# Kernel tuning notes

Hardware: AMD Instinct MI355X
Metric: run time of the kernel (lower is better)

The kernel has to match this reference:

```python
import jax, jax.numpy as jnp
import numpy as np

D_MODEL = 1024
NUM_HEADS = 16
D_K = D_MODEL // NUM_HEADS


def setup_inputs() -> dict:
    key = jax.random.key(0)
    ks = jax.random.split(key, 9)
    s = 1.0 / np.sqrt(D_MODEL)
    x = jax.random.normal(ks[0], (2, 2048, D_MODEL), dtype=jnp.float32)
    Wq = jax.random.uniform(ks[1], (D_MODEL, D_MODEL), jnp.float32, -s, s)
    bq = jax.random.uniform(ks[2], (D_MODEL,), jnp.float32, -s, s)
    Wk = jax.random.uniform(ks[3], (D_MODEL, D_MODEL), jnp.float32, -s, s)
    bk = jax.random.uniform(ks[4], (D_MODEL,), jnp.float32, -s, s)
    Wv = jax.random.uniform(ks[5], (D_MODEL, D_MODEL), jnp.float32, -s, s)
    bv = jax.random.uniform(ks[6], (D_MODEL,), jnp.float32, -s, s)
    Wo = jax.random.uniform(ks[7], (D_MODEL, D_MODEL), jnp.float32, -s, s)
    bo = jax.random.uniform(ks[8], (D_MODEL,), jnp.float32, -s, s)
    return {"x": x, "Wq": Wq, "bq": bq, "Wk": Wk, "bk": bk,
            "Wv": Wv, "bv": bv, "Wo": Wo, "bo": bo}


def reference(x, Wq, bq, Wk, bk, Wv, bv, Wo, bo):
    B, S, _ = x.shape
    # projections (torch Linear: x @ W.T + b; here W stored as [in, out])
    q = (x @ Wq + bq).reshape(B, S, NUM_HEADS, D_K).transpose(0, 2, 1, 3)
    k = (x @ Wk + bk).reshape(B, S, NUM_HEADS, D_K).transpose(0, 2, 1, 3)
    v = (x @ Wv + bv).reshape(B, S, NUM_HEADS, D_K).transpose(0, 2, 1, 3)
    scores = jnp.einsum('bhqd,bhkd->bhqk', q, k) / jnp.sqrt(jnp.float32(D_K))
    attn = jax.nn.softmax(scores, axis=-1)
    out = jnp.einsum('bhqk,bhkd->bhqd', attn, v)  # [B,H,S,Dk]
    out = out.transpose(0, 2, 1, 3).reshape(B, S, D_MODEL)
    return out @ Wo + bo
```

## Files before the change

kernel.cpp:

```cpp
#include <hip/hip_runtime.h>
#include <hip/hip_bf16.h>

#define SEQ   2048
#define DM    1024
#define NH    16
#define DK    64
#define BATCH 2
#define M_TOT 4096
#define C1 0.18033688011112042f

typedef __attribute__((ext_vector_type(8))) short bf16x8;
typedef __attribute__((ext_vector_type(4))) float f32x4;
typedef __attribute__((ext_vector_type(16))) float f32x16;
typedef __attribute__((ext_vector_type(2))) int i32x2;
typedef unsigned short u16;

__device__ inline u16 f2b(float f) {
    union { float f; unsigned u; } x; x.f = f;
    return (u16)((x.u + 0x7FFFu + ((x.u >> 16) & 1u)) >> 16);
}

__device__ inline unsigned pk2(float a, float b) {
    __hip_bfloat162 h = __float22bfloat162_rn(make_float2(a, b));
    return *reinterpret_cast<unsigned*>(&h);
}

__device__ inline void async_cp16(const u16* g, u16* l) {
    __builtin_amdgcn_global_load_lds(
        (const __attribute__((address_space(1))) unsigned int*)g,
        (__attribute__((address_space(3))) unsigned int*)l, 16, 0, 0);
}

__device__ inline f32x16 zero16() {
    f32x16 z;
    #pragma unroll
    for (int i = 0; i < 16; ++i) z[i] = 0.f;
    return z;
}

__device__ inline bf16x8 mk8(unsigned a, unsigned b, unsigned c, unsigned d) {
    union { unsigned u[4]; bf16x8 v; } x;
    x.u[0] = a; x.u[1] = b; x.u[2] = c; x.u[3] = d;
    return x.v;
}

#define MFMA32(a, b, c) __builtin_amdgcn_mfma_f32_32x32x16_bf16(a, b, c, 0, 0, 0)

__global__ __launch_bounds__(256) void cast_x(
    const float4* __restrict__ x, uint2* __restrict__ xb)
{
    int gid = blockIdx.x * 256 + threadIdx.x;
    float4 v = x[gid];
    uint2 o;
    o.x = pk2(v.x, v.y); o.y = pk2(v.z, v.w);
    xb[gid] = o;
}

__global__ __launch_bounds__(256) void transpose_cast4(
    const float* __restrict__ W0, const float* __restrict__ W1,
    const float* __restrict__ W2, const float* __restrict__ W3,
    u16* __restrict__ WtBase)
{
    __shared__ float tile[32][33];
    const int t = threadIdx.x;
    const int n0 = blockIdx.x << 5, k0 = blockIdx.y << 5, z = blockIdx.z;
    const float* W = (z == 0) ? W0 : (z == 1) ? W1 : (z == 2) ? W2 : W3;
    u16* Wt = WtBase + (size_t)z * DM * DM;
    #pragma unroll
    for (int i = 0; i < 4; ++i) {
        int idx = t + (i << 8); int r = idx >> 5, c = idx & 31;
        tile[r][c] = W[(size_t)(k0 + r) * DM + n0 + c];
    }
    __syncthreads();
    #pragma unroll
    for (int i = 0; i < 4; ++i) {
        int idx = t + (i << 8); int r = idx >> 5, c = idx & 31;
        Wt[(size_t)(n0 + r) * DM + k0 + c] = f2b(tile[c][r]);
    }
}

__global__ __launch_bounds__(256) void gemm_bt(
    const u16* __restrict__ A, const u16* __restrict__ Bt, int mode,
    const float* __restrict__ bias0, const float* __restrict__ bias1,
    const float* __restrict__ bias2,
    void* __restrict__ out0, void* __restrict__ out1, void* __restrict__ out2)
{
    __shared__ u16 sh[9216];
    u16* As = sh;
    u16* Bs = sh + 4096;
    const int t = threadIdx.x, wid = t >> 6, lane = t & 63;
    const int lr = lane & 15, quad = lane >> 4;
    const int m0 = blockIdx.y << 7, n0 = blockIdx.x << 7;
    const int wm = (wid & 1) << 6, wn = (wid >> 1) << 6;
    const int rowA = lane >> 2;
    const int colA = (((lane & 3) - ((lane >> 3) & 3)) & 3) << 3;
    const int sA = (((lr >> 1) + quad) & 3) << 3;

    f32x4 acc[4][4];
    #pragma unroll
    for (int i = 0; i < 4; ++i)
        #pragma unroll
        for (int j = 0; j < 4; ++j) acc[i][j] = (f32x4){0.f, 0.f, 0.f, 0.f};

    for (int k0 = 0; k0 < DM; k0 += 32) {
        #pragma unroll
        for (int i = 0; i < 2; ++i) {
            int ch = wid * 2 + i;
            async_cp16(A  + (size_t)(m0 + ch * 16 + rowA) * DM + k0 + colA,
                       As + ch * 16 * 32);
            async_cp16(Bt + (size_t)(n0 + ch * 16 + rowA) * DM + k0 + colA,
                       Bs + ch * 16 * 32);
        }
        __syncthreads();
        bf16x8 af[4], bfr[4];
        #pragma unroll
        for (int mt = 0; mt < 4; ++mt)
            af[mt] = *(const bf16x8*)(As + (wm + 16 * mt + lr) * 32 + sA);
        #pragma unroll
        for (int nt = 0; nt < 4; ++nt)
            bfr[nt] = *(const bf16x8*)(Bs + (wn + 16 * nt + lr) * 32 + sA);
        #pragma unroll
        for (int mt = 0; mt < 4; ++mt)
            #pragma unroll
            for (int nt = 0; nt < 4; ++nt)
                acc[mt][nt] = __builtin_amdgcn_mfma_f32_16x16x32_bf16(
                    af[mt], bfr[nt], acc[mt][nt], 0, 0, 0);
        __syncthreads();
    }

    if (mode == 1) {
        u16* wstrip = sh + wid * 1152;
        const int ngb = n0 + wn;
        const int which = ngb >> 10, nnb = ngb & 1023;
        const int h = nnb >> 6;
        const float* bp = (which == 0) ? bias0 : (which == 1) ? bias1 : bias2;
        const float sc = (which == 0) ? C1 : 1.0f;
        float bias_v[4];
        #pragma unroll
        for (int nt = 0; nt < 4; ++nt) bias_v[nt] = bp[nnb + 16 * nt + lr];

        if (which != 1) {
            u16* dst = (which == 0) ? (u16*)out0 : (u16*)out2;
            #pragma unroll
            for (int mt = 0; mt < 4; ++mt) {
                #pragma unroll
                for (int nt = 0; nt < 4; ++nt) {
                    uint2 w;
                    w.x = pk2((acc[mt][nt][0] + bias_v[nt]) * sc,
                              (acc[mt][nt][1] + bias_v[nt]) * sc);
                    w.y = pk2((acc[mt][nt][2] + bias_v[nt]) * sc,
                              (acc[mt][nt][3] + bias_v[nt]) * sc);
                    *(uint2*)(wstrip + (16 * nt + lr) * 16 + quad * 4) = w;
                }
                asm volatile("s_waitcnt lgkmcnt(0)" ::: "memory");
                #pragma unroll
                for (int half = 0; half < 2; ++half) {
                    int id = lane + 64 * half;
                    int d = id >> 1, cho = (id & 1) << 3;
                    int m = m0 + wm + 16 * mt + cho;
                    int b = m >> 11, s = m & (SEQ - 1);
                    *(uint4*)(dst + ((size_t)(b * NH + h) * DK + d) * SEQ + s) =
                        *(const uint4*)(wstrip + d * 16 + cho);
                }
                asm volatile("s_waitcnt lgkmcnt(0)" ::: "memory");
            }
        } else {
            u16* dst = (u16*)out1;
            #pragma unroll
            for (int mt = 0; mt < 4; ++mt) {
                #pragma unroll
                for (int nt = 0; nt < 4; ++nt)
                    #pragma unroll
                    for (int r = 0; r < 4; ++r)
                        wstrip[(quad * 4 + r) * 72 + 16 * nt + lr] =
                            f2b(acc[mt][nt][r] + bias_v[nt]);
                asm volatile("s_waitcnt lgkmcnt(0)" ::: "memory");
                #pragma unroll
                for (int half = 0; half < 2; ++half) {
                    int id = lane + 64 * half;
                    int mloc = id >> 3, dl = (id & 7) << 3;
                    int m = m0 + wm + 16 * mt + mloc;
                    int b = m >> 11, s = m & (SEQ - 1);
                    *(uint4*)(dst + ((size_t)(b * NH + h) * SEQ + s) * DK + dl) =
                        *(const uint4*)(wstrip + mloc * 72 + dl);
                }
                asm volatile("s_waitcnt lgkmcnt(0)" ::: "memory");
            }
        }
    } else {
        float* O = (float*)out0;
        float* strip = (float*)sh + wid * 1088;
        float bias_v[4];
        #pragma unroll
        for (int nt = 0; nt < 4; ++nt) bias_v[nt] = bias0[n0 + wn + 16 * nt + lr];
        #pragma unroll
        for (int mt = 0; mt < 4; ++mt) {
            #pragma unroll
            for (int nt = 0; nt < 4; ++nt)
                #pragma unroll
                for (int r = 0; r < 4; ++r)
                    strip[(quad * 4 + r) * 68 + 16 * nt + lr] =
                        acc[mt][nt][r] + bias_v[nt];
            asm volatile("s_waitcnt lgkmcnt(0)" ::: "memory");
            #pragma unroll
            for (int rr = 0; rr < 4; ++rr) {
                int row = lane >> 2, chunk = (lane & 3) + 4 * rr;
                float4 v = *(const float4*)(strip + row * 68 + chunk * 4);
                *(float4*)(O + (size_t)(m0 + wm + 16 * mt + row) * DM
                             + n0 + wn + chunk * 4) = v;
            }
            asm volatile("s_waitcnt lgkmcnt(0)" ::: "memory");
        }
    }
}

__global__ __launch_bounds__(256) void attn_mfma(
    const u16* __restrict__ Qt, const u16* __restrict__ K,
    const u16* __restrict__ Vt, u16* __restrict__ A)
{
    __shared__ u16 sh[16640];

    const int t = threadIdx.x, wid = t >> 6, lane = t & 63;
    const int l31 = lane & 31, hi = lane >> 5, l7 = lane & 7;
    const int bx = blockIdx.x;
    const int xcd = bx & 7, within = bx >> 3;
    const int bh  = xcd * 4 + (within >> 4);
    const int q0  = (within & 15) << 7;

    const u16* Kb = K  + (size_t)bh * SEQ * DK;
    const u16* Vb = Vt + (size_t)bh * DK * SEQ;

    const int qw = q0 + 32 * wid + l31;
    const u16* Qb = Qt + (size_t)bh * DK * SEQ + qw;
    bf16x8 bQ[4];
    #pragma unroll
    for (int s = 0; s < 4; ++s)
        #pragma unroll
        for (int j = 0; j < 8; ++j)
            bQ[s][j] = (short)Qb[(size_t)(16 * s + 8 * hi + j) * SEQ];

    f32x16 O0 = zero16(), O1 = zero16();
    float lr = 0.f;

    const int srow = t >> 3;
    const int scol = (((t & 7) ^ (srow & 7)) << 3);

    const int rA = l31 * 64;
    int cks[4];
    #pragma unroll
    for (int s = 0; s < 4; ++s) cks[s] = ((2 * s + hi) ^ l7) << 3;

    auto stage = [&](int kt, int buf) {
        u16* kd = sh + (buf << 12);
        u16* vd = sh + 8192 + (buf << 12);
        async_cp16(Kb + (size_t)(kt + srow) * DK + scol,       kd + wid * 512);
        async_cp16(Kb + (size_t)(kt + srow + 32) * DK + scol,  kd + 2048 + wid * 512);
        async_cp16(Vb + (size_t)srow * SEQ + kt + scol,        vd + wid * 512);
        async_cp16(Vb + (size_t)(srow + 32) * SEQ + kt + scol, vd + 2048 + wid * 512);
    };

    stage(0, 0);
    __syncthreads();

    for (int it = 0; it < SEQ / 64; ++it) {
        const u16* kbp = sh + ((it & 1) << 12) + rA;
        const u16* vbp = sh + 8192 + ((it & 1) << 12) + rA;
        if (it + 1 < SEQ / 64) stage((it + 1) << 6, (it + 1) & 1);

        f32x16 Sv[2];
        __builtin_amdgcn_s_setprio(1);
        {
            bf16x8 a;
            f32x16 s0 = zero16();
            a = *(const bf16x8*)(kbp + cks[0]); s0 = MFMA32(a, bQ[0], s0);
            a = *(const bf16x8*)(kbp + cks[1]); s0 = MFMA32(a, bQ[1], s0);
            a = *(const bf16x8*)(kbp + cks[2]); s0 = MFMA32(a, bQ[2], s0);
            a = *(const bf16x8*)(kbp + cks[3]); s0 = MFMA32(a, bQ[3], s0);
            Sv[0] = s0;
            f32x16 s1 = zero16();
            a = *(const bf16x8*)(kbp + 2048 + cks[0]); s1 = MFMA32(a, bQ[0], s1);
            a = *(const bf16x8*)(kbp + 2048 + cks[1]); s1 = MFMA32(a, bQ[1], s1);
            a = *(const bf16x8*)(kbp + 2048 + cks[2]); s1 = MFMA32(a, bQ[2], s1);
            a = *(const bf16x8*)(kbp + 2048 + cks[3]); s1 = MFMA32(a, bQ[3], s1);
            Sv[1] = s1;
        }
        __builtin_amdgcn_s_setprio(0);

        unsigned pa[4][4];
        #pragma unroll
        for (int kvt = 0; kvt < 2; ++kvt) {
            float e[16];
            #pragma unroll
            for (int r = 0; r < 16; ++r)
                e[r] = __builtin_amdgcn_exp2f(Sv[kvt][r]);
            lr += (((e[0] + e[1]) + (e[2] + e[3])) +
                   ((e[4] + e[5]) + (e[6] + e[7]))) +
                  (((e[8] + e[9]) + (e[10] + e[11])) +
                   ((e[12] + e[13]) + (e[14] + e[15])));
            unsigned pk8[8];
            #pragma unroll
            for (int i = 0; i < 8; ++i) pk8[i] = pk2(e[2 * i], e[2 * i + 1]);
            #pragma unroll
            for (int ww = 0; ww < 2; ++ww) {
                i32x2 r0 = __builtin_amdgcn_permlane32_swap(
                    (int)pk8[4 * ww + 0], (int)pk8[4 * ww + 2], false, false);
                i32x2 r1 = __builtin_amdgcn_permlane32_swap(
                    (int)pk8[4 * ww + 1], (int)pk8[4 * ww + 3], false, false);
                const int w = 2 * kvt + ww;
                pa[w][0] = (unsigned)r0[0]; pa[w][1] = (unsigned)r1[0];
                pa[w][2] = (unsigned)r0[1]; pa[w][3] = (unsigned)r1[1];
            }
        }

        __builtin_amdgcn_s_setprio(1);
        #pragma unroll
        for (int w = 0; w < 4; ++w) {
            bf16x8 pw = mk8(pa[w][0], pa[w][1], pa[w][2], pa[w][3]);
            bf16x8 v0 = *(const bf16x8*)(vbp + cks[w]);
            bf16x8 v1 = *(const bf16x8*)(vbp + 2048 + cks[w]);
            O0 = MFMA32(pw, v0, O0);
            O1 = MFMA32(pw, v1, O1);
        }
        __builtin_amdgcn_s_setprio(0);

        __syncthreads();
    }

    lr += __shfl_xor(lr, 32);
    float* lt = (float*)(sh + 16384) + wid * 32;
    lt[l31] = lr;
    asm volatile("s_waitcnt lgkmcnt(0)" ::: "memory");

    const int b = bh >> 4, h = bh & 15;
    u16* Ab = A + (size_t)b * SEQ * DM + h * DK + l31;
    #pragma unroll
    for (int r = 0; r < 16; ++r) {
        const int qr = (r & 3) + 8 * (r >> 2) + 4 * hi;
        const float inv = 1.f / lt[qr];
        u16* dst = Ab + (size_t)(q0 + 32 * wid + qr) * DM;
        dst[0]  = f2b(O0[r] * inv);
        dst[32] = f2b(O1[r] * inv);
    }
}

extern "C" void kernel_launch(void* const* d_in, const int* in_sizes, int n_in,
                              void* d_out, int out_size, void* d_ws, size_t ws_size,
                              hipStream_t stream)
{
    const float* x  = (const float*)d_in[0];
    const float* Wq = (const float*)d_in[1];
    const float* bq = (const float*)d_in[2];
    const float* Wk = (const float*)d_in[3];
    const float* bk = (const float*)d_in[4];
    const float* Wv = (const float*)d_in[5];
    const float* bv = (const float*)d_in[6];
    const float* Wo = (const float*)d_in[7];
    const float* bo = (const float*)d_in[8];

    const size_t NE = (size_t)M_TOT * DM;
    u16* xb     = (u16*)d_ws;
    u16* wt_qkv = xb + NE;
    u16* wt_o   = wt_qkv + 3 * (size_t)DM * DM;
    u16* qt_ws  = wt_o + (size_t)DM * DM;
    u16* k_ws   = qt_ws + NE;
    u16* vt_ws  = k_ws + NE;
    u16* a_ws   = vt_ws + NE;

    cast_x<<<M_TOT * DM / 4 / 256, 256, 0, stream>>>((const float4*)x, (uint2*)xb);
    transpose_cast4<<<dim3(32, 32, 4), 256, 0, stream>>>(Wq, Wk, Wv, Wo, wt_qkv);

    gemm_bt<<<dim3(24, 32), 256, 0, stream>>>(
        xb, wt_qkv, 1, bq, bk, bv, qt_ws, k_ws, vt_ws);

    attn_mfma<<<dim3(512), 256, 0, stream>>>(qt_ws, k_ws, vt_ws, a_ws);

    gemm_bt<<<dim3(8, 32), 256, 0, stream>>>(
        a_ws, wt_o, 0, bo, nullptr, nullptr, d_out, nullptr, nullptr);
}
```

Before: 211.0 us.

## Split attention KV sequence across two wave groups with LDS reduction

The attention block grows to 512 threads: two groups of four waves each process alternating 64-key halves of a 128-key stage, so each block stages twice as much K/V per iteration and runs half as many loop iterations. At the end, group 1 writes its partial O and row sums to LDS and group 0 adds them and writes the normalized output. This doubles in-flight waves per query tile to hide MFMA/exp latency, at the cost of double the LDS and a final cross-group reduction.

```diff
diff --git a/kernel.cpp b/kernel.cpp
--- a/kernel.cpp
+++ b/kernel.cpp
@@ -214,14 +214,15 @@
     }
 }
 
-__global__ __launch_bounds__(256) void attn_mfma(
+__global__ __launch_bounds__(512) void attn_mfma(
     const u16* __restrict__ Qt, const u16* __restrict__ K,
     const u16* __restrict__ Vt, u16* __restrict__ A)
 {
-    __shared__ u16 sh[16640];
+    __shared__ u16 sh[33280];
 
     const int t = threadIdx.x, wid = t >> 6, lane = t & 63;
     const int l31 = lane & 31, hi = lane >> 5, l7 = lane & 7;
+    const int g = wid >> 2, wq = wid & 3;
     const int bx = blockIdx.x;
     const int xcd = bx & 7, within = bx >> 3;
     const int bh  = xcd * 4 + (within >> 4);
@@ -230,7 +231,7 @@
     const u16* Kb = K  + (size_t)bh * SEQ * DK;
     const u16* Vb = Vt + (size_t)bh * DK * SEQ;
 
-    const int qw = q0 + 32 * wid + l31;
+    const int qw = q0 + 32 * wq + l31;
     const u16* Qb = Qt + (size_t)bh * DK * SEQ + qw;
     bf16x8 bQ[4];
     #pragma unroll
@@ -242,47 +243,46 @@
     f32x16 O0 = zero16(), O1 = zero16();
     float lr = 0.f;
 
-    const int srow = t >> 3;
-    const int scol = (((t & 7) ^ (srow & 7)) << 3);
+    const int w8row = wid * 8 + (lane >> 3);
+    const int scol  = ((l7 ^ (lane >> 3)) << 3);
 
     const int rA = l31 * 64;
     int cks[4];
     #pragma unroll
     for (int s = 0; s < 4; ++s) cks[s] = ((2 * s + hi) ^ l7) << 3;
 
-    auto stage = [&](int kt, int buf) {
-        u16* kd = sh + (buf << 12);
-        u16* vd = sh + 8192 + (buf << 12);
-        async_cp16(Kb + (size_t)(kt + srow) * DK + scol,       kd + wid * 512);
-        async_cp16(Kb + (size_t)(kt + srow + 32) * DK + scol,  kd + 2048 + wid * 512);
-        async_cp16(Vb + (size_t)srow * SEQ + kt + scol,        vd + wid * 512);
-        async_cp16(Vb + (size_t)(srow + 32) * SEQ + kt + scol, vd + 2048 + wid * 512);
+    auto stage = [&](int sit, int buf) {
+        const int kt = sit << 7;
+        u16* kd = sh + (buf << 13) + wid * 512;
+        u16* vd = sh + 16384 + (buf << 13) + wid * 512;
+        async_cp16(Kb + (size_t)(kt + w8row) * DK + scol,       kd);
+        async_cp16(Kb + (size_t)(kt + 64 + w8row) * DK + scol,  kd + 4096);
+        async_cp16(Vb + (size_t)w8row * SEQ + kt + scol,        vd);
+        async_cp16(Vb + (size_t)w8row * SEQ + kt + 64 + scol,   vd + 4096);
     };
 
     stage(0, 0);
     __syncthreads();
 
-    for (int it = 0; it < SEQ / 64; ++it) {
-        const u16* kbp = sh + ((it & 1) << 12) + rA;
-        const u16* vbp = sh + 8192 + ((it & 1) << 12) + rA;
-        if (it + 1 < SEQ / 64) stage((it + 1) << 6, (it + 1) & 1);
+    for (int sit = 0; sit < SEQ / 128; ++sit) {
+        const u16* kbp = sh + ((sit & 1) << 13) + (g << 12) + rA;
+        const u16* vbp = sh + 16384 + ((sit & 1) << 13) + (g << 12) + rA;
+        if (sit + 1 < SEQ / 128) stage(sit + 1, (sit + 1) & 1);
 
         f32x16 Sv[2];
         __builtin_amdgcn_s_setprio(1);
         {
             bf16x8 a;
-            f32x16 s0 = zero16();
-            a = *(const bf16x8*)(kbp + cks[0]); s0 = MFMA32(a, bQ[0], s0);
-            a = *(const bf16x8*)(kbp + cks[1]); s0 = MFMA32(a, bQ[1], s0);
-            a = *(const bf16x8*)(kbp + cks[2]); s0 = MFMA32(a, bQ[2], s0);
-            a = *(const bf16x8*)(kbp + cks[3]); s0 = MFMA32(a, bQ[3], s0);
-            Sv[0] = s0;
-            f32x16 s1 = zero16();
-            a = *(const bf16x8*)(kbp + 2048 + cks[0]); s1 = MFMA32(a, bQ[0], s1);
-            a = *(const bf16x8*)(kbp + 2048 + cks[1]); s1 = MFMA32(a, bQ[1], s1);
-            a = *(const bf16x8*)(kbp + 2048 + cks[2]); s1 = MFMA32(a, bQ[2], s1);
-            a = *(const bf16x8*)(kbp + 2048 + cks[3]); s1 = MFMA32(a, bQ[3], s1);
-            Sv[1] = s1;
+            Sv[0] = zero16();
+            a = *(const bf16x8*)(kbp + cks[0]); Sv[0] = MFMA32(a, bQ[0], Sv[0]);
+            a = *(const bf16x8*)(kbp + cks[1]); Sv[0] = MFMA32(a, bQ[1], Sv[0]);
+            a = *(const bf16x8*)(kbp + cks[2]); Sv[0] = MFMA32(a, bQ[2], Sv[0]);
+            a = *(const bf16x8*)(kbp + cks[3]); Sv[0] = MFMA32(a, bQ[3], Sv[0]);
+            Sv[1] = zero16();
+            a = *(const bf16x8*)(kbp + 2048 + cks[0]); Sv[1] = MFMA32(a, bQ[0], Sv[1]);
+            a = *(const bf16x8*)(kbp + 2048 + cks[1]); Sv[1] = MFMA32(a, bQ[1], Sv[1]);
+            a = *(const bf16x8*)(kbp + 2048 + cks[2]); Sv[1] = MFMA32(a, bQ[2], Sv[1]);
+            a = *(const bf16x8*)(kbp + 2048 + cks[3]); Sv[1] = MFMA32(a, bQ[3], Sv[1]);
         }
         __builtin_amdgcn_s_setprio(0);
 
@@ -327,19 +327,46 @@
     }
 
     lr += __shfl_xor(lr, 32);
-    float* lt = (float*)(sh + 16384) + wid * 32;
-    lt[l31] = lr;
-    asm volatile("s_waitcnt lgkmcnt(0)" ::: "memory");
-
-    const int b = bh >> 4, h = bh & 15;
-    u16* Ab = A + (size_t)b * SEQ * DM + h * DK + l31;
-    #pragma unroll
-    for (int r = 0; r < 16; ++r) {
-        const int qr = (r & 3) + 8 * (r >> 2) + 4 * hi;
-        const float inv = 1.f / lt[qr];
-        u16* dst = Ab + (size_t)(q0 + 32 * wid + qr) * DM;
-        dst[0]  = f2b(O0[r] * inv);
-        dst[32] = f2b(O1[r] * inv);
+
+    float* lred = (float*)(sh + 32768);
+    if (g == 1) {
+        float* red = (float*)sh + wq * 2048;
+        #pragma unroll
+        for (int c = 0; c < 4; ++c) {
+            float4 v0 = make_float4(O0[4*c], O0[4*c+1], O0[4*c+2], O0[4*c+3]);
+            float4 v1 = make_float4(O1[4*c], O1[4*c+1], O1[4*c+2], O1[4*c+3]);
+            *(float4*)(red + lane * 32 + ((c ^ l7) << 2))       = v0;
+            *(float4*)(red + lane * 32 + (((c + 4) ^ l7) << 2)) = v1;
+        }
+        if (hi == 0) lred[wq * 32 + l31] = lr;
+    }
+    __syncthreads();
+
+    if (g == 0) {
+        float* red = (float*)sh + wq * 2048;
+        #pragma unroll
+        for (int c = 0; c < 4; ++c) {
+            float4 v0 = *(const float4*)(red + lane * 32 + ((c ^ l7) << 2));
+            float4 v1 = *(const float4*)(red + lane * 32 + (((c + 4) ^ l7) << 2));
+            O0[4*c] += v0.x; O0[4*c+1] += v0.y; O0[4*c+2] += v0.z; O0[4*c+3] += v0.w;
+            O1[4*c] += v1.x; O1[4*c+1] += v1.y; O1[4*c+2] += v1.z; O1[4*c+3] += v1.w;
+        }
+        lr += lred[wq * 32 + l31];
+
+        float* lt = (float*)(sh + 33024) + wq * 32;
+        lt[l31] = lr;
+        asm volatile("s_waitcnt lgkmcnt(0)" ::: "memory");
+
+        const int b = bh >> 4, h = bh & 15;
+        u16* Ab = A + (size_t)b * SEQ * DM + h * DK + l31;
+        #pragma unroll
+        for (int r = 0; r < 16; ++r) {
+            const int qr = (r & 3) + 8 * (r >> 2) + 4 * hi;
+            const float inv = 1.f / lt[qr];
+            u16* dst = Ab + (size_t)(q0 + 32 * wq + qr) * DM;
+            dst[0]  = f2b(O0[r] * inv);
+            dst[32] = f2b(O1[r] * inv);
+        }
     }
 }
 
@@ -372,7 +399,7 @@
     gemm_bt<<<dim3(24, 32), 256, 0, stream>>>(
         xb, wt_qkv, 1, bq, bk, bv, qt_ws, k_ws, vt_ws);
 
-    attn_mfma<<<dim3(512), 256, 0, stream>>>(qt_ws, k_ws, vt_ws, a_ws);
+    attn_mfma<<<dim3(512), 512, 0, stream>>>(qt_ws, k_ws, vt_ws, a_ws);
 
     gemm_bt<<<dim3(8, 32), 256, 0, stream>>>(
         a_ws, wt_o, 0, bo, nullptr, nullptr, d_out, nullptr, nullptr);
```

Result: faster. 200.3 us (-5.1%).
